# Kernel tuning notes

Measured on AMD Instinct MI355X. Metric: run time of the kernel, lower is better.

The kernel has to match this reference:

```python
import jax, jax.numpy as jnp
import numpy as np

A, U, ANT, D2, H = 128, 8, 64, 64, 256
NUE = A * U            # 1024 ues
E_INT = A * NUE        # 131072 interferes edges (all ap x ue pairs)
E_DL = NUE             # one d_link edge per ue


def _mlp(x, Wa, ba, Wb, bb):
    return jax.nn.relu(x @ Wa + ba) @ Wb + bb


def setup_inputs() -> dict:
    key = jax.random.key(0)
    ks = jax.random.split(key, 14)
    f32 = jnp.float32
    inp = {
        'pl_int_re': jax.random.normal(ks[0], (E_INT, ANT), f32) * 0.1,
        'pl_int_im': jax.random.normal(ks[1], (E_INT, ANT), f32) * 0.1,
        'pl_dl_re': jax.random.normal(ks[2], (E_DL, ANT), f32) * 0.1,
        'pl_dl_im': jax.random.normal(ks[3], (E_DL, ANT), f32) * 0.1,
        'pv_re': jax.random.normal(ks[4], (A, U, ANT), f32) * 0.1,
        'pv_im': jax.random.normal(ks[5], (A, U, ANT), f32) * 0.1,
        'W2a': jax.random.normal(ks[6], (4 * ANT, H), f32) / np.sqrt(4 * ANT),
        'b2a': jnp.zeros((H,), f32),
        'W2b': jax.random.normal(ks[7], (H, D2), f32) / np.sqrt(H),
        'b2b': jnp.zeros((D2,), f32),
        'W1a': jax.random.normal(ks[8], (1 + 2 * ANT + D2, H), f32) / np.sqrt(1 + 2 * ANT + D2),
        'b1a': jnp.zeros((H,), f32),
        'W1b': jax.random.normal(ks[9], (H, 2 * ANT), f32) / np.sqrt(H),
        'b1b': jnp.zeros((2 * ANT,), f32),
        # interferes: every ap -> every ue
        'int_src': jnp.repeat(jnp.arange(A, dtype=jnp.int32), NUE),
        'int_dst': jnp.tile(jnp.arange(NUE, dtype=jnp.int32), A),
        # d_link: ap a -> ues [a*U, (a+1)*U)
        'dl_src': jnp.repeat(jnp.arange(A, dtype=jnp.int32), U),
        'dl_dst': jnp.arange(NUE, dtype=jnp.int32),
    }
    return inp


def reference(pl_int_re, pl_int_im, pl_dl_re, pl_dl_im, pv_re, pv_im,
              W2a, b2a, W2b, b2b, W1a, b1a, W1b, b1b,
              int_src, int_dst, dl_src, dl_dst):
    pv = jax.lax.complex(pv_re, pv_im)            # [A,U,ANT] ap power_vector
    pl_int = jax.lax.complex(pl_int_re, pl_int_im)  # [E_INT,ANT]
    pl_dl = jax.lax.complex(pl_dl_re, pl_dl_im)     # [E_DL,ANT]

    def aggregate_interferes(pv_cur):
        src_sum = jnp.sum(pv_cur, axis=1)[int_src]              # [E,ANT]
        infer_vec = src_sum.conj() * pl_int                      # [E,ANT]
        sum_ap = jnp.sum(jnp.abs(infer_vec) ** 2, axis=-1)       # ||.||^2 -> [E]
        return jax.ops.segment_sum(sum_ap[:, None], int_dst, num_segments=NUE)  # [NUE,1]

    # 1) aggregate_interferes (stored in graph; recomputed at the end)
    _ = aggregate_interferes(pv)

    # 2) mlp_aggregate_interferes
    src_sum = jnp.sum(pv, axis=1)[int_src]                       # [E,ANT] complex
    feats = jnp.concatenate([pl_int, src_sum], axis=1)           # [E,2*ANT] complex
    cat_feats = jnp.concatenate([feats.real, feats.imag], axis=1)  # [E,4*ANT]
    msg2 = _mlp(cat_feats, W2a, b2a, W2b, b2b)                   # [E,D2]
    mlp_ue_all = jax.ops.segment_sum(msg2, int_dst, num_segments=NUE)  # [NUE,D2]

    # 3) update_ue_power_vector (d_link edges)
    src_pv_dl = pv[dl_src]                                       # [E_DL,U,ANT]
    iner = jnp.einsum('eua,ea->eu', src_pv_dl.conj(), pl_dl)     # bmm -> [E_DL,U]
    norm1 = jnp.abs(iner) ** 2                                   # [E_DL,U]
    mask1 = jnp.ones((E_DL, U), norm1.dtype).at[jnp.arange(E_DL), dl_dst % U].set(0.0)
    in_infer = jnp.sum(norm1 * mask1, axis=1)[:, None]           # [E_DL,1]

    feat1 = jnp.concatenate([in_infer, pl_dl.real, pl_dl.imag, mlp_ue_all[dl_dst]], axis=1)
    out1 = _mlp(feat1, W1a, b1a, W1b, b1b).reshape(E_DL, 2, ANT)  # [E_DL,2,ANT]
    ue_pv_msg = jax.lax.complex(out1[:, 0, :], out1[:, 1, :])    # [E_DL,ANT]
    # each ue receives exactly one message
    ue_pv = jnp.zeros((NUE, ANT), ue_pv_msg.dtype).at[dl_dst].set(ue_pv_msg)

    # 4) update_ap_power_vector (u_link: ue i -> ap i//U; mailbox [A,U,ANT])
    mailbox = ue_pv.reshape(A, U, ANT)
    flat = mailbox.reshape(A, U * ANT)
    row_sums = jnp.sum(jnp.abs(flat), axis=-1, keepdims=True)
    pv_new = (flat / row_sums).reshape(A, U, ANT)

    # 5) final aggregate_interferes with updated power vectors
    ue_all_interference = aggregate_interferes(pv_new)

    out_stacked = jnp.stack([pv_new.real, pv_new.imag])          # [2,A,U,ANT]
    return out_stacked, ue_all_interference
```

## Files before the change

### kernel.cpp

```cpp
#include <hip/hip_runtime.h>
#include <hip/hip_bf16.h>
#include <hip/hip_fp16.h>

#define A_NUM 128
#define U_NUM 8
#define ANT 64
#define D2 64
#define H_DIM 256
#define NUE 1024
#define E_INT 131072

typedef __attribute__((ext_vector_type(8))) short bf16x8_t;
typedef __attribute__((ext_vector_type(4))) short bf16x4_t;
typedef __attribute__((ext_vector_type(4))) float f32x4_t;

static __device__ inline unsigned short f2bf(float x) {
    unsigned int u = __float_as_uint(x);
    unsigned int r = (u + 0x7fffu + ((u >> 16) & 1u)) >> 16;
    return (unsigned short)r;
}
static __device__ inline unsigned int pack2(float a, float b) {
    return (unsigned int)f2bf(a) | ((unsigned int)f2bf(b) << 16);
}
static __device__ inline unsigned int packh2(float a, float b) {
    return (unsigned int)__half_as_ushort(__float2half(a)) |
           ((unsigned int)__half_as_ushort(__float2half(b)) << 16);
}
static __device__ inline bf16x4_t relu_cvt4(f32x4_t v) {
    float t0 = v[0] > 0.f ? v[0] : 0.f;
    float t1 = v[1] > 0.f ? v[1] : 0.f;
    float t2 = v[2] > 0.f ? v[2] : 0.f;
    float t3 = v[3] > 0.f ? v[3] : 0.f;
    union { unsigned int u[2]; bf16x4_t s; } r;
    r.u[0] = pack2(t0, t1);
    r.u[1] = pack2(t2, t3);
    return r.s;
}

__global__ void prep_kernel(const float* __restrict__ pv_re, const float* __restrict__ pv_im,
                            const float* __restrict__ W2a, const float* __restrict__ b2a,
                            const float* __restrict__ W2b,
                            const float* __restrict__ W1a, const float* __restrict__ W1b,
                            float* __restrict__ Sa, unsigned short* __restrict__ WpF,
                            unsigned short* __restrict__ W2F,
                            float* __restrict__ W1aT, float* __restrict__ W1bT) {
    int bid = blockIdx.x, t = threadIdx.x;
    if (bid < A_NUM) {
        __shared__ float sre[ANT], sim[ANT];
        if (t < ANT) {
            float s = 0.f;
            for (int u = 0; u < U_NUM; ++u) s += pv_re[bid * 512 + u * 64 + t];
            sre[t] = s;
        } else if (t < 2 * ANT) {
            int ant = t - ANT;
            float s = 0.f;
            for (int u = 0; u < U_NUM; ++u) s += pv_im[bid * 512 + u * 64 + ant];
            sim[ant] = s;
        }
        __syncthreads();
        float a0 = 0.f, a1 = 0.f, a2 = 0.f, a3 = 0.f;
        for (int ant = 0; ant < ANT; ant += 2) {
            a0 += sre[ant] * W2a[(64 + ant) * H_DIM + t];
            a1 += sim[ant] * W2a[(192 + ant) * H_DIM + t];
            a2 += sre[ant + 1] * W2a[(64 + ant + 1) * H_DIM + t];
            a3 += sim[ant + 1] * W2a[(192 + ant + 1) * H_DIM + t];
        }
        Sa[bid * H_DIM + t] = b2a[t] + ((a0 + a2) + (a1 + a3));
    } else if (bid < 136) {
        int base = (bid - A_NUM) * 256 + t;
        for (int f = base; f < 32768 + 16384; f += 8 * 256) {
            if (f < 32768) {
                int i = f & 7, lml = (f >> 3) & 15, lkl = (f >> 7) & 3;
                int kc = (f >> 9) & 3, ht8 = (f >> 11) & 7, hh = (f >> 14) & 1;
                int h = hh * 128 + ht8 * 16 + lml;
                int k = kc * 32 + lkl * 8 + i;
                int row = (k < 64) ? k : (k + 64);
                WpF[f] = f2bf(W2a[row * H_DIM + h]);
            } else {
                int f2 = f - 32768;
                int i = f2 & 3, ll = (f2 >> 2) & 63;
                int dt = (f2 >> 8) & 3, ht8 = (f2 >> 10) & 7, hh = (f2 >> 13) & 1;
                int d = dt * 16 + (ll & 15);
                int k = hh * 128 + ht8 * 16 + (ll >> 4) * 4 + i;
                W2F[f2] = f2bf(W2b[k * D2 + d]);
            }
        }
    } else {
        for (int i = (bid - 136) * 256 + t; i < 53248 + 32768; i += 32 * 256) {
            if (i < 53248) {
                int k = i >> 8, h = i & 255;
                W1aT[h * 208 + k] = (k < 193) ? W1a[k * 256 + h] : 0.f;
            } else {
                int i2 = i - 53248;
                int k = i2 >> 7, c = i2 & 127;
                W1bT[c * 256 + k] = W1b[k * 128 + c];
            }
        }
    }
}

__global__ __launch_bounds__(512) void mlp2_kernel(
        const float* __restrict__ plre, const float* __restrict__ plim,
        const float* __restrict__ Sa, const unsigned short* __restrict__ WpF,
        const unsigned short* __restrict__ W2F, float* __restrict__ partial,
        unsigned short* __restrict__ Pws) {
    __shared__ __attribute__((aligned(16))) unsigned short Wl[16384];
    __shared__ __attribute__((aligned(16))) unsigned short W2l[8192];
    __shared__ __attribute__((aligned(16))) unsigned short Fbuf[8704];
    int bid = blockIdx.x;
    int ac = bid >> 5, hh = (bid >> 4) & 1, jtile = bid & 15;
    int j0 = jtile * 64, a0 = ac * 8;
    int t = threadIdx.x, l = t & 63, lm = l & 15, lk = l >> 4;
    int wv = t >> 6, jw = wv >> 2, hw = wv & 3;

    {
        const uint4* sW = reinterpret_cast<const uint4*>(WpF + hh * 16384);
        const uint4* sW2 = reinterpret_cast<const uint4*>(W2F + hh * 8192);
        uint4* dW = reinterpret_cast<uint4*>(Wl);
        uint4* dW2 = reinterpret_cast<uint4*>(W2l);
        for (int q = t; q < 3072; q += 512) {
            if (q < 2048) dW[q] = sW[q];
            else dW2[q - 2048] = sW2[q - 2048];
        }
    }

    int er = t >> 3, sg = t & 7;
    const float* sb = (sg < 4) ? plre : plim;
    int soff = (j0 + er) * 64 + (sg & 3) * 16;
    int fw = er * 136 + ((sg < 4) ? 0 : 64) + (sg & 3) * 16;

    f32x4_t acc2[4][2];
#pragma unroll
    for (int dt = 0; dt < 4; ++dt)
#pragma unroll
        for (int jt = 0; jt < 2; ++jt) acc2[dt][jt] = (f32x4_t){0.f, 0.f, 0.f, 0.f};

    float4 s0, s1, s2, s3;
    {
        const float* p = sb + (size_t)a0 * 65536 + soff;
        s0 = *reinterpret_cast<const float4*>(p);
        s1 = *reinterpret_cast<const float4*>(p + 4);
        s2 = *reinterpret_cast<const float4*>(p + 8);
        s3 = *reinterpret_cast<const float4*>(p + 12);
        *reinterpret_cast<uint4*>(&Fbuf[fw]) =
            make_uint4(pack2(s0.x, s0.y), pack2(s0.z, s0.w),
                       pack2(s1.x, s1.y), pack2(s1.z, s1.w));
        *reinterpret_cast<uint4*>(&Fbuf[fw + 8]) =
            make_uint4(pack2(s2.x, s2.y), pack2(s2.z, s2.w),
                       pack2(s3.x, s3.y), pack2(s3.z, s3.w));
    }
    {
        const float* p = sb + (size_t)(a0 + 1) * 65536 + soff;
        s0 = *reinterpret_cast<const float4*>(p);
        s1 = *reinterpret_cast<const float4*>(p + 4);
        s2 = *reinterpret_cast<const float4*>(p + 8);
        s3 = *reinterpret_cast<const float4*>(p + 12);
    }
    __syncthreads();

    for (int ai = 0; ai < 8; ++ai) {
        int a = a0 + ai;
        if (hh == 0) {
            uint4 rr = *reinterpret_cast<const uint4*>(Fbuf + er * 136 + sg * 8);
            uint4 ri = *reinterpret_cast<const uint4*>(Fbuf + er * 136 + 64 + sg * 8);
            const unsigned short* pr = (const unsigned short*)&rr;
            const unsigned short* pi = (const unsigned short*)&ri;
            unsigned int pk[4];
#pragma unroll
            for (int i = 0; i < 4; ++i) {
                float re0 = __uint_as_float(((unsigned int)pr[2 * i]) << 16);
                float im0 = __uint_as_float(((unsigned int)pi[2 * i]) << 16);
                float re1 = __uint_as_float(((unsigned int)pr[2 * i + 1]) << 16);
                float im1 = __uint_as_float(((unsigned int)pi[2 * i + 1]) << 16);
                pk[i] = packh2(re0 * re0 + im0 * im0, re1 * re1 + im1 * im1);
            }
            *reinterpret_cast<uint4*>(&Pws[(unsigned)(a * 1024 + j0 + er) * 64 + sg * 8]) =
                make_uint4(pk[0], pk[1], pk[2], pk[3]);
        }
        f32x4_t acc1[2][2];
#pragma unroll
        for (int ht = 0; ht < 2; ++ht) {
            f32x4_t sa = *reinterpret_cast<const f32x4_t*>(
                Sa + a * H_DIM + hh * 128 + hw * 32 + ht * 16 + lk * 4);
            acc1[ht][0] = sa;
            acc1[ht][1] = sa;
        }
#pragma unroll
        for (int kc = 0; kc < 4; ++kc) {
            bf16x8_t aw0 = *reinterpret_cast<const bf16x8_t*>(
                Wl + (((hw * 2 + 0) * 4 + kc) << 9) + l * 8);
            bf16x8_t aw1 = *reinterpret_cast<const bf16x8_t*>(
                Wl + (((hw * 2 + 1) * 4 + kc) << 9) + l * 8);
            bf16x8_t bf0 = *reinterpret_cast<const bf16x8_t*>(
                Fbuf + (jw * 32 + lm) * 136 + kc * 32 + lk * 8);
            bf16x8_t bf1 = *reinterpret_cast<const bf16x8_t*>(
                Fbuf + (jw * 32 + 16 + lm) * 136 + kc * 32 + lk * 8);
            acc1[0][0] = __builtin_amdgcn_mfma_f32_16x16x32_bf16(aw0, bf0, acc1[0][0], 0, 0, 0);
            acc1[0][1] = __builtin_amdgcn_mfma_f32_16x16x32_bf16(aw0, bf1, acc1[0][1], 0, 0, 0);
            acc1[1][0] = __builtin_amdgcn_mfma_f32_16x16x32_bf16(aw1, bf0, acc1[1][0], 0, 0, 0);
            acc1[1][1] = __builtin_amdgcn_mfma_f32_16x16x32_bf16(aw1, bf1, acc1[1][1], 0, 0, 0);
        }
#pragma unroll
        for (int ht = 0; ht < 2; ++ht) {
            bf16x4_t hl0 = relu_cvt4(acc1[ht][0]);
            bf16x4_t hl1 = relu_cvt4(acc1[ht][1]);
#pragma unroll
            for (int dt = 0; dt < 4; ++dt) {
                bf16x4_t w2 = *reinterpret_cast<const bf16x4_t*>(
                    W2l + (((hw * 2 + ht) * 4 + dt) << 8) + l * 4);
                acc2[dt][0] = __builtin_amdgcn_mfma_f32_16x16x16bf16_1k(w2, hl0, acc2[dt][0], 0, 0, 0);
                acc2[dt][1] = __builtin_amdgcn_mfma_f32_16x16x16bf16_1k(w2, hl1, acc2[dt][1], 0, 0, 0);
            }
        }
        if (ai < 7) {
            __syncthreads();
            *reinterpret_cast<uint4*>(&Fbuf[fw]) =
                make_uint4(pack2(s0.x, s0.y), pack2(s0.z, s0.w),
                           pack2(s1.x, s1.y), pack2(s1.z, s1.w));
            *reinterpret_cast<uint4*>(&Fbuf[fw + 8]) =
                make_uint4(pack2(s2.x, s2.y), pack2(s2.z, s2.w),
                           pack2(s3.x, s3.y), pack2(s3.z, s3.w));
            if (ai < 6) {
                const float* p = sb + (size_t)(a0 + ai + 2) * 65536 + soff;
                s0 = *reinterpret_cast<const float4*>(p);
                s1 = *reinterpret_cast<const float4*>(p + 4);
                s2 = *reinterpret_cast<const float4*>(p + 8);
                s3 = *reinterpret_cast<const float4*>(p + 12);
            }
            __syncthreads();
        }
    }

    float* R = reinterpret_cast<float*>(Fbuf);
#define STORE_R()                                                              \
    do {                                                                       \
        _Pragma("unroll") for (int dt = 0; dt < 4; ++dt)                       \
            _Pragma("unroll") for (int jt = 0; jt < 2; ++jt)                   \
                *reinterpret_cast<f32x4_t*>(                                   \
                    &R[(jw * 32 + jt * 16 + lm) * 68 + dt * 16 + lk * 4]) =    \
                    acc2[dt][jt];                                              \
    } while (0)
#define ADD_R()                                                                \
    do {                                                                       \
        _Pragma("unroll") for (int dt = 0; dt < 4; ++dt)                       \
            _Pragma("unroll") for (int jt = 0; jt < 2; ++jt)                   \
                acc2[dt][jt] += *reinterpret_cast<const f32x4_t*>(             \
                    &R[(jw * 32 + jt * 16 + lm) * 68 + dt * 16 + lk * 4]);     \
    } while (0)
    __syncthreads();
    if (hw == 1) STORE_R();
    __syncthreads();
    if (hw == 0) ADD_R();
    __syncthreads();
    if (hw == 3) STORE_R();
    __syncthreads();
    if (hw == 2) ADD_R();
    __syncthreads();
    if (hw == 2) STORE_R();
    __syncthreads();
    if (hw == 0) {
        ADD_R();
#pragma unroll
        for (int dt = 0; dt < 4; ++dt)
#pragma unroll
            for (int jt = 0; jt < 2; ++jt)
                *reinterpret_cast<float4*>(
                    &partial[(size_t)(hh * 16 + ac) * 65536 +
                             (j0 + jw * 32 + jt * 16 + lm) * 64 + dt * 16 + lk * 4]) =
                    *reinterpret_cast<float4*>(&acc2[dt][jt]);
    }
#undef STORE_R
#undef ADD_R
}

__global__ __launch_bounds__(512) void dlink_norm(
        const float* __restrict__ pv_re, const float* __restrict__ pv_im,
        const float* __restrict__ pldre, const float* __restrict__ pldim,
        const float* __restrict__ partial, const float* __restrict__ b2b,
        const float* __restrict__ W1aT, const float* __restrict__ b1a,
        const float* __restrict__ W1bT, const float* __restrict__ b1b,
        float* __restrict__ Q, float* __restrict__ out) {
    int a = blockIdx.x, t = threadIdx.x, w = t >> 6, l = t & 63;
    __shared__ float pvr[512], pvi[512], pldr[512], pldi[512];
    __shared__ float nrm[8][8];
    __shared__ __attribute__((aligned(16))) float feat[8][212];
    __shared__ __attribute__((aligned(16))) float h1[8][260];
    __shared__ float red2[2][8][128];
    __shared__ __attribute__((aligned(16))) float o1[8][128];
    __shared__ float redn[8];
    __shared__ float SshInv;

    pvr[t] = pv_re[a * 512 + t];
    pvi[t] = pv_im[a * 512 + t];
    pldr[t] = pldre[a * 512 + t];
    pldi[t] = pldim[a * 512 + t];
    {
        float acc = 128.f * b2b[t & 63];
#pragma unroll
        for (int c = 0; c < 32; ++c) acc += partial[c * 65536 + a * 512 + t];
        feat[t >> 6][129 + (t & 63)] = acc;
    }
    if (t < 152) feat[t / 19][193 + t % 19] = 0.f;
    __syncthreads();
    feat[t >> 6][1 + (t & 63)] = pldr[t];
    feat[t >> 6][65 + (t & 63)] = pldi[t];
#pragma unroll
    for (int p = 0; p < 8; ++p) {
        int idx = w * 8 + p;
        int el = idx >> 3, u = idx & 7;
        float pr = pvr[u * 64 + l], pi = pvi[u * 64 + l];
        float qr = pldr[el * 64 + l], qi = pldi[el * 64 + l];
        float ir = pr * qr + pi * qi;
        float ii = pr * qi - pi * qr;
        for (int m = 1; m < 64; m <<= 1) {
            ir += __shfl_xor(ir, m, 64);
            ii += __shfl_xor(ii, m, 64);
        }
        if (l == 0) nrm[el][u] = ir * ir + ii * ii;
    }
    __syncthreads();
    if (t < 8) {
        float s = 0.f;
        for (int u = 0; u < 8; ++u)
            if (u != t) s += nrm[t][u];
        feat[t][0] = s;
    }
    __syncthreads();
    {
        int h = t >> 1, e0 = (t & 1) * 4;
        const float4* wrow = reinterpret_cast<const float4*>(W1aT + h * 208);
        const float4* f0p = reinterpret_cast<const float4*>(&feat[e0 + 0][0]);
        const float4* f1p = reinterpret_cast<const float4*>(&feat[e0 + 1][0]);
        const float4* f2p = reinterpret_cast<const float4*>(&feat[e0 + 2][0]);
        const float4* f3p = reinterpret_cast<const float4*>(&feat[e0 + 3][0]);
        float ac0 = 0.f, ac1 = 0.f, ac2 = 0.f, ac3 = 0.f;
#pragma unroll 4
        for (int kq = 0; kq < 52; ++kq) {
            float4 wv = wrow[kq];
            float4 f0 = f0p[kq], f1 = f1p[kq], f2 = f2p[kq], f3 = f3p[kq];
            ac0 = fmaf(wv.x, f0.x, ac0); ac0 = fmaf(wv.y, f0.y, ac0);
            ac0 = fmaf(wv.z, f0.z, ac0); ac0 = fmaf(wv.w, f0.w, ac0);
            ac1 = fmaf(wv.x, f1.x, ac1); ac1 = fmaf(wv.y, f1.y, ac1);
            ac1 = fmaf(wv.z, f1.z, ac1); ac1 = fmaf(wv.w, f1.w, ac1);
            ac2 = fmaf(wv.x, f2.x, ac2); ac2 = fmaf(wv.y, f2.y, ac2);
            ac2 = fmaf(wv.z, f2.z, ac2); ac2 = fmaf(wv.w, f2.w, ac2);
            ac3 = fmaf(wv.x, f3.x, ac3); ac3 = fmaf(wv.y, f3.y, ac3);
            ac3 = fmaf(wv.w, f3.w, ac3); ac3 = fmaf(wv.z, f3.z, ac3);
        }
        float bb = b1a[h];
        float s0 = bb + ac0, s1 = bb + ac1, s2 = bb + ac2, s3 = bb + ac3;
        h1[e0 + 0][h] = s0 > 0.f ? s0 : 0.f;
        h1[e0 + 1][h] = s1 > 0.f ? s1 : 0.f;
        h1[e0 + 2][h] = s2 > 0.f ? s2 : 0.f;
        h1[e0 + 3][h] = s3 > 0.f ? s3 : 0.f;
    }
    __syncthreads();
    {
        int e0 = (t & 1) * 4, c = (t >> 1) & 127, kh = t >> 8;
        const float4* wrow = reinterpret_cast<const float4*>(W1bT + c * 256 + kh * 128);
        const float4* g0 = reinterpret_cast<const float4*>(&h1[e0 + 0][kh * 128]);
        const float4* g1 = reinterpret_cast<const float4*>(&h1[e0 + 1][kh * 128]);
        const float4* g2 = reinterpret_cast<const float4*>(&h1[e0 + 2][kh * 128]);
        const float4* g3 = reinterpret_cast<const float4*>(&h1[e0 + 3][kh * 128]);
        float ac0 = 0.f, ac1 = 0.f, ac2 = 0.f, ac3 = 0.f;
#pragma unroll 4
        for (int kq = 0; kq < 32; ++kq) {
            float4 wv = wrow[kq];
            float4 f0 = g0[kq], f1 = g1[kq], f2 = g2[kq], f3 = g3[kq];
            ac0 = fmaf(wv.x, f0.x, ac0); ac0 = fmaf(wv.y, f0.y, ac0);
            ac0 = fmaf(wv.z, f0.z, ac0); ac0 = fmaf(wv.w, f0.w, ac0);
            ac1 = fmaf(wv.x, f1.x, ac1); ac1 = fmaf(wv.y, f1.y, ac1);
            ac1 = fmaf(wv.z, f1.z, ac1); ac1 = fmaf(wv.w, f1.w, ac1);
            ac2 = fmaf(wv.x, f2.x, ac2); ac2 = fmaf(wv.y, f2.y, ac2);
            ac2 = fmaf(wv.z, f2.z, ac2); ac2 = fmaf(wv.w, f2.w, ac2);
            ac3 = fmaf(wv.x, f3.x, ac3); ac3 = fmaf(wv.y, f3.y, ac3);
            ac3 = fmaf(wv.z, f3.z, ac3); ac3 = fmaf(wv.w, f3.w, ac3);
        }
        red2[kh][e0 + 0][c] = ac0;
        red2[kh][e0 + 1][c] = ac1;
        red2[kh][e0 + 2][c] = ac2;
        red2[kh][e0 + 3][c] = ac3;
    }
    __syncthreads();
    {
        int i0 = t, i1 = t + 512;
        o1[i0 >> 7][i0 & 127] = b1b[i0 & 127] + red2[0][i0 >> 7][i0 & 127] + red2[1][i0 >> 7][i0 & 127];
        o1[i1 >> 7][i1 & 127] = b1b[i1 & 127] + red2[0][i1 >> 7][i1 & 127] + red2[1][i1 >> 7][i1 & 127];
    }
    __syncthreads();
    {
        int el = t >> 6, ant = t & 63;
        float re = o1[el][ant], im = o1[el][64 + ant];
        float v = sqrtf(re * re + im * im);
        for (int m = 1; m < 64; m <<= 1) v += __shfl_xor(v, m, 64);
        if (l == 0) redn[w] = v;
    }
    __syncthreads();
    if (t == 0) {
        float S = redn[0] + redn[1] + redn[2] + redn[3] +
                  redn[4] + redn[5] + redn[6] + redn[7];
        SshInv = 1.f / S;
    }
    __syncthreads();
    {
        float inv = SshInv;
        int el = t >> 6, ant = t & 63;
        out[a * 512 + t] = o1[el][ant] * inv;
        out[65536 + a * 512 + t] = o1[el][64 + ant] * inv;
        if (t < 64) {
            float sr = 0.f, si = 0.f;
#pragma unroll
            for (int u = 0; u < 8; ++u) {
                sr += o1[u][t];
                si += o1[u][64 + t];
            }
            sr *= inv;
            si *= inv;
            Q[a * 64 + t] = sr * sr + si * si;
        }
    }
}

__global__ __launch_bounds__(256) void final_agg(const unsigned short* __restrict__ Pws,
                                                 const float* __restrict__ Qv,
                                                 float* __restrict__ out) {
    int bid = blockIdx.x, t = threadIdx.x, w = t >> 6, l = t & 63;
    __shared__ __attribute__((aligned(16))) float Qc[128][68];
    for (int i = t; i < 8192; i += 256) Qc[i >> 6][i & 63] = Qv[i];
    __syncthreads();
    int j = bid * 4 + w;
    int as = l >> 3, og = l & 7;
    float acc = 0.f;
#pragma unroll 4
    for (int ab = 0; ab < 16; ++ab) {
        int aa = ab * 8 + as;
        uint4 pv4 = *reinterpret_cast<const uint4*>(&Pws[(unsigned)(aa * 1024 + j) * 64 + og * 8]);
        float4 q0 = *reinterpret_cast<const float4*>(&Qc[aa][og * 8]);
        float4 q1 = *reinterpret_cast<const float4*>(&Qc[aa][og * 8 + 4]);
        const unsigned short* hp = (const unsigned short*)&pv4;
        acc += __half2float(__ushort_as_half(hp[0])) * q0.x;
        acc += __half2float(__ushort_as_half(hp[1])) * q0.y;
        acc += __half2float(__ushort_as_half(hp[2])) * q0.z;
        acc += __half2float(__ushort_as_half(hp[3])) * q0.w;
        acc += __half2float(__ushort_as_half(hp[4])) * q1.x;
        acc += __half2float(__ushort_as_half(hp[5])) * q1.y;
        acc += __half2float(__ushort_as_half(hp[6])) * q1.z;
        acc += __half2float(__ushort_as_half(hp[7])) * q1.w;
    }
    for (int m = 1; m < 64; m <<= 1) acc += __shfl_xor(acc, m, 64);
    if (l == 0) out[131072 + j] = acc;
}

extern "C" void kernel_launch(void* const* d_in, const int* in_sizes, int n_in,
                              void* d_out, int out_size, void* d_ws, size_t ws_size,
                              hipStream_t stream) {
    const float* plre = (const float*)d_in[0];
    const float* plim = (const float*)d_in[1];
    const float* pldre = (const float*)d_in[2];
    const float* pldim = (const float*)d_in[3];
    const float* pvre = (const float*)d_in[4];
    const float* pvim = (const float*)d_in[5];
    const float* W2a = (const float*)d_in[6];
    const float* b2a = (const float*)d_in[7];
    const float* W2b = (const float*)d_in[8];
    const float* b2b = (const float*)d_in[9];
    const float* W1a = (const float*)d_in[10];
    const float* b1a = (const float*)d_in[11];
    const float* W1b = (const float*)d_in[12];
    const float* b1b = (const float*)d_in[13];

    char* ws = (char*)d_ws;
    float* Sa = (float*)(ws);
    unsigned short* WpF = (unsigned short*)(ws + 131072);
    unsigned short* W2F = (unsigned short*)(ws + 196608);
    float* Q = (float*)(ws + 229376);
    float* W1aT = (float*)(ws + 262144);
    float* W1bT = (float*)(ws + 475136);
    float* partial = (float*)(ws + 606208);
    unsigned short* Pws = (unsigned short*)(ws + 8994816);
    float* out = (float*)d_out;

    prep_kernel<<<168, 256, 0, stream>>>(pvre, pvim, W2a, b2a, W2b, W1a, W1b,
                                         Sa, WpF, W2F, W1aT, W1bT);
    mlp2_kernel<<<512, 512, 0, stream>>>(plre, plim, Sa, WpF, W2F, partial, Pws);
    dlink_norm<<<128, 512, 0, stream>>>(pvre, pvim, pldre, pldim, partial, b2b,
                                        W1aT, b1a, W1bT, b1b, Q, out);
    final_agg<<<256, 256, 0, stream>>>(Pws, Q, out);
}
```

Baseline: 66.22 us.

## Halve mlp2 block to 256 threads with each wave covering all 64 edge rows

The mlp2 kernel now runs 4 waves per block instead of 8. Each wave handles all four 16-row edge fragments instead of two, so every weight fragment loaded from LDS feeds twice as many MFMAs. Each thread now loads and converts twice as much of the input tile, and holds twice as many accumulators, which raises register pressure and may cut occupancy. It also reorders two FMAs in dlink_norm, which slightly changes the floating-point summation order.

```diff
diff --git a/kernel.cpp b/kernel.cpp
--- a/kernel.cpp
+++ b/kernel.cpp
@@ -99,7 +99,7 @@
     }
 }
 
-__global__ __launch_bounds__(512) void mlp2_kernel(
+__global__ __launch_bounds__(256) void mlp2_kernel(
         const float* __restrict__ plre, const float* __restrict__ plim,
         const float* __restrict__ Sa, const unsigned short* __restrict__ WpF,
         const unsigned short* __restrict__ W2F, float* __restrict__ partial,
@@ -111,79 +111,87 @@
     int ac = bid >> 5, hh = (bid >> 4) & 1, jtile = bid & 15;
     int j0 = jtile * 64, a0 = ac * 8;
     int t = threadIdx.x, l = t & 63, lm = l & 15, lk = l >> 4;
-    int wv = t >> 6, jw = wv >> 2, hw = wv & 3;
+    int hw = t >> 6;
 
     {
         const uint4* sW = reinterpret_cast<const uint4*>(WpF + hh * 16384);
         const uint4* sW2 = reinterpret_cast<const uint4*>(W2F + hh * 8192);
         uint4* dW = reinterpret_cast<uint4*>(Wl);
         uint4* dW2 = reinterpret_cast<uint4*>(W2l);
-        for (int q = t; q < 3072; q += 512) {
+        for (int q = t; q < 3072; q += 256) {
             if (q < 2048) dW[q] = sW[q];
             else dW2[q - 2048] = sW2[q - 2048];
         }
     }
 
-    int er = t >> 3, sg = t & 7;
-    const float* sb = (sg < 4) ? plre : plim;
-    int soff = (j0 + er) * 64 + (sg & 3) * 16;
-    int fw = er * 136 + ((sg < 4) ? 0 : 64) + (sg & 3) * 16;
-
-    f32x4_t acc2[4][2];
+    int rr = t >> 2, seg = t & 3;
+    const float* sb = (seg < 2) ? plre : plim;
+    int soff = (j0 + rr) * 64 + (seg & 1) * 32;
+    int fw = rr * 136 + ((seg < 2) ? 0 : 64) + (seg & 1) * 32;
+
+    f32x4_t acc2[4][4];
 #pragma unroll
     for (int dt = 0; dt < 4; ++dt)
 #pragma unroll
-        for (int jt = 0; jt < 2; ++jt) acc2[dt][jt] = (f32x4_t){0.f, 0.f, 0.f, 0.f};
-
-    float4 s0, s1, s2, s3;
+        for (int jf = 0; jf < 4; ++jf) acc2[dt][jf] = (f32x4_t){0.f, 0.f, 0.f, 0.f};
+
+    float4 s[8];
     {
         const float* p = sb + (size_t)a0 * 65536 + soff;
-        s0 = *reinterpret_cast<const float4*>(p);
-        s1 = *reinterpret_cast<const float4*>(p + 4);
-        s2 = *reinterpret_cast<const float4*>(p + 8);
-        s3 = *reinterpret_cast<const float4*>(p + 12);
-        *reinterpret_cast<uint4*>(&Fbuf[fw]) =
-            make_uint4(pack2(s0.x, s0.y), pack2(s0.z, s0.w),
-                       pack2(s1.x, s1.y), pack2(s1.z, s1.w));
-        *reinterpret_cast<uint4*>(&Fbuf[fw + 8]) =
-            make_uint4(pack2(s2.x, s2.y), pack2(s2.z, s2.w),
-                       pack2(s3.x, s3.y), pack2(s3.z, s3.w));
+#pragma unroll
+        for (int i = 0; i < 8; ++i) s[i] = *reinterpret_cast<const float4*>(p + i * 4);
+#pragma unroll
+        for (int i = 0; i < 4; ++i)
+            *reinterpret_cast<uint4*>(&Fbuf[fw + i * 8]) =
+                make_uint4(pack2(s[2 * i].x, s[2 * i].y), pack2(s[2 * i].z, s[2 * i].w),
+                           pack2(s[2 * i + 1].x, s[2 * i + 1].y), pack2(s[2 * i + 1].z, s[2 * i + 1].w));
     }
     {
         const float* p = sb + (size_t)(a0 + 1) * 65536 + soff;
-        s0 = *reinterpret_cast<const float4*>(p);
-        s1 = *reinterpret_cast<const float4*>(p + 4);
-        s2 = *reinterpret_cast<const float4*>(p + 8);
-        s3 = *reinterpret_cast<const float4*>(p + 12);
+#pragma unroll
+        for (int i = 0; i < 8; ++i) s[i] = *reinterpret_cast<const float4*>(p + i * 4);
     }
     __syncthreads();
 
     for (int ai = 0; ai < 8; ++ai) {
         int a = a0 + ai;
         if (hh == 0) {
-            uint4 rr = *reinterpret_cast<const uint4*>(Fbuf + er * 136 + sg * 8);
-            uint4 ri = *reinterpret_cast<const uint4*>(Fbuf + er * 136 + 64 + sg * 8);
-            const unsigned short* pr = (const unsigned short*)&rr;
-            const unsigned short* pi = (const unsigned short*)&ri;
-            unsigned int pk[4];
+            uint4 re0 = *reinterpret_cast<const uint4*>(Fbuf + rr * 136 + seg * 16);
+            uint4 re1 = *reinterpret_cast<const uint4*>(Fbuf + rr * 136 + seg * 16 + 8);
+            uint4 im0 = *reinterpret_cast<const uint4*>(Fbuf + rr * 136 + 64 + seg * 16);
+            uint4 im1 = *reinterpret_cast<const uint4*>(Fbuf + rr * 136 + 64 + seg * 16 + 8);
+            const unsigned short* pr = (const unsigned short*)&re0;
+            const unsigned short* pi = (const unsigned short*)&im0;
+            unsigned int pk[8];
 #pragma unroll
             for (int i = 0; i < 4; ++i) {
-                float re0 = __uint_as_float(((unsigned int)pr[2 * i]) << 16);
-                float im0 = __uint_as_float(((unsigned int)pi[2 * i]) << 16);
-                float re1 = __uint_as_float(((unsigned int)pr[2 * i + 1]) << 16);
-                float im1 = __uint_as_float(((unsigned int)pi[2 * i + 1]) << 16);
-                pk[i] = packh2(re0 * re0 + im0 * im0, re1 * re1 + im1 * im1);
-            }
-            *reinterpret_cast<uint4*>(&Pws[(unsigned)(a * 1024 + j0 + er) * 64 + sg * 8]) =
-                make_uint4(pk[0], pk[1], pk[2], pk[3]);
-        }
-        f32x4_t acc1[2][2];
+                float a0f = __uint_as_float(((unsigned int)pr[2 * i]) << 16);
+                float b0f = __uint_as_float(((unsigned int)pi[2 * i]) << 16);
+                float a1f = __uint_as_float(((unsigned int)pr[2 * i + 1]) << 16);
+                float b1f = __uint_as_float(((unsigned int)pi[2 * i + 1]) << 16);
+                pk[i] = packh2(a0f * a0f + b0f * b0f, a1f * a1f + b1f * b1f);
+            }
+            pr = (const unsigned short*)&re1;
+            pi = (const unsigned short*)&im1;
+#pragma unroll
+            for (int i = 0; i < 4; ++i) {
+                float a0f = __uint_as_float(((unsigned int)pr[2 * i]) << 16);
+                float b0f = __uint_as_float(((unsigned int)pi[2 * i]) << 16);
+                float a1f = __uint_as_float(((unsigned int)pr[2 * i + 1]) << 16);
+                float b1f = __uint_as_float(((unsigned int)pi[2 * i + 1]) << 16);
+                pk[4 + i] = packh2(a0f * a0f + b0f * b0f, a1f * a1f + b1f * b1f);
+            }
+            unsigned short* pd = Pws + (unsigned)(a * 1024 + j0 + rr) * 64 + seg * 16;
+            *reinterpret_cast<uint4*>(pd) = make_uint4(pk[0], pk[1], pk[2], pk[3]);
+            *reinterpret_cast<uint4*>(pd + 8) = make_uint4(pk[4], pk[5], pk[6], pk[7]);
+        }
+        f32x4_t acc1[2][4];
 #pragma unroll
         for (int ht = 0; ht < 2; ++ht) {
             f32x4_t sa = *reinterpret_cast<const f32x4_t*>(
                 Sa + a * H_DIM + hh * 128 + hw * 32 + ht * 16 + lk * 4);
-            acc1[ht][0] = sa;
-            acc1[ht][1] = sa;
+#pragma unroll
+            for (int jf = 0; jf < 4; ++jf) acc1[ht][jf] = sa;
         }
 #pragma unroll
         for (int kc = 0; kc < 4; ++kc) {
@@ -191,41 +199,39 @@
                 Wl + (((hw * 2 + 0) * 4 + kc) << 9) + l * 8);
             bf16x8_t aw1 = *reinterpret_cast<const bf16x8_t*>(
                 Wl + (((hw * 2 + 1) * 4 + kc) << 9) + l * 8);
-            bf16x8_t bf0 = *reinterpret_cast<const bf16x8_t*>(
-                Fbuf + (jw * 32 + lm) * 136 + kc * 32 + lk * 8);
-            bf16x8_t bf1 = *reinterpret_cast<const bf16x8_t*>(
-                Fbuf + (jw * 32 + 16 + lm) * 136 + kc * 32 + lk * 8);
-            acc1[0][0] = __builtin_amdgcn_mfma_f32_16x16x32_bf16(aw0, bf0, acc1[0][0], 0, 0, 0);
-            acc1[0][1] = __builtin_amdgcn_mfma_f32_16x16x32_bf16(aw0, bf1, acc1[0][1], 0, 0, 0);
-            acc1[1][0] = __builtin_amdgcn_mfma_f32_16x16x32_bf16(aw1, bf0, acc1[1][0], 0, 0, 0);
-            acc1[1][1] = __builtin_amdgcn_mfma_f32_16x16x32_bf16(aw1, bf1, acc1[1][1], 0, 0, 0);
+#pragma unroll
+            for (int jf = 0; jf < 4; ++jf) {
+                bf16x8_t bf = *reinterpret_cast<const bf16x8_t*>(
+                    Fbuf + (jf * 16 + lm) * 136 + kc * 32 + lk * 8);
+                acc1[0][jf] = __builtin_amdgcn_mfma_f32_16x16x32_bf16(aw0, bf, acc1[0][jf], 0, 0, 0);
+                acc1[1][jf] = __builtin_amdgcn_mfma_f32_16x16x32_bf16(aw1, bf, acc1[1][jf], 0, 0, 0);
+            }
         }
 #pragma unroll
         for (int ht = 0; ht < 2; ++ht) {
-            bf16x4_t hl0 = relu_cvt4(acc1[ht][0]);
-            bf16x4_t hl1 = relu_cvt4(acc1[ht][1]);
+            bf16x4_t hl[4];
+#pragma unroll
+            for (int jf = 0; jf < 4; ++jf) hl[jf] = relu_cvt4(acc1[ht][jf]);
 #pragma unroll
             for (int dt = 0; dt < 4; ++dt) {
                 bf16x4_t w2 = *reinterpret_cast<const bf16x4_t*>(
                     W2l + (((hw * 2 + ht) * 4 + dt) << 8) + l * 4);
-                acc2[dt][0] = __builtin_amdgcn_mfma_f32_16x16x16bf16_1k(w2, hl0, acc2[dt][0], 0, 0, 0);
-                acc2[dt][1] = __builtin_amdgcn_mfma_f32_16x16x16bf16_1k(w2, hl1, acc2[dt][1], 0, 0, 0);
+#pragma unroll
+                for (int jf = 0; jf < 4; ++jf)
+                    acc2[dt][jf] = __builtin_amdgcn_mfma_f32_16x16x16bf16_1k(w2, hl[jf], acc2[dt][jf], 0, 0, 0);
             }
         }
         if (ai < 7) {
             __syncthreads();
-            *reinterpret_cast<uint4*>(&Fbuf[fw]) =
-                make_uint4(pack2(s0.x, s0.y), pack2(s0.z, s0.w),
-                           pack2(s1.x, s1.y), pack2(s1.z, s1.w));
-            *reinterpret_cast<uint4*>(&Fbuf[fw + 8]) =
-                make_uint4(pack2(s2.x, s2.y), pack2(s2.z, s2.w),
-                           pack2(s3.x, s3.y), pack2(s3.z, s3.w));
+#pragma unroll
+            for (int i = 0; i < 4; ++i)
+                *reinterpret_cast<uint4*>(&Fbuf[fw + i * 8]) =
+                    make_uint4(pack2(s[2 * i].x, s[2 * i].y), pack2(s[2 * i].z, s[2 * i].w),
+                               pack2(s[2 * i + 1].x, s[2 * i + 1].y), pack2(s[2 * i + 1].z, s[2 * i + 1].w));
             if (ai < 6) {
                 const float* p = sb + (size_t)(a0 + ai + 2) * 65536 + soff;
-                s0 = *reinterpret_cast<const float4*>(p);
-                s1 = *reinterpret_cast<const float4*>(p + 4);
-                s2 = *reinterpret_cast<const float4*>(p + 8);
-                s3 = *reinterpret_cast<const float4*>(p + 12);
+#pragma unroll
+                for (int i = 0; i < 8; ++i) s[i] = *reinterpret_cast<const float4*>(p + i * 4);
             }
             __syncthreads();
         }
@@ -235,17 +241,16 @@
 #define STORE_R()                                                              \
     do {                                                                       \
         _Pragma("unroll") for (int dt = 0; dt < 4; ++dt)                       \
-            _Pragma("unroll") for (int jt = 0; jt < 2; ++jt)                   \
+            _Pragma("unroll") for (int jf = 0; jf < 4; ++jf)                   \
                 *reinterpret_cast<f32x4_t*>(                                   \
-                    &R[(jw * 32 + jt * 16 + lm) * 68 + dt * 16 + lk * 4]) =    \
-                    acc2[dt][jt];                                              \
+                    &R[(jf * 16 + lm) * 68 + dt * 16 + lk * 4]) = acc2[dt][jf];\
     } while (0)
 #define ADD_R()                                                                \
     do {                                                                       \
         _Pragma("unroll") for (int dt = 0; dt < 4; ++dt)                       \
-            _Pragma("unroll") for (int jt = 0; jt < 2; ++jt)                   \
-                acc2[dt][jt] += *reinterpret_cast<const f32x4_t*>(             \
-                    &R[(jw * 32 + jt * 16 + lm) * 68 + dt * 16 + lk * 4]);     \
+            _Pragma("unroll") for (int jf = 0; jf < 4; ++jf)                   \
+                acc2[dt][jf] += *reinterpret_cast<const f32x4_t*>(             \
+                    &R[(jf * 16 + lm) * 68 + dt * 16 + lk * 4]);               \
     } while (0)
     __syncthreads();
     if (hw == 1) STORE_R();
@@ -263,11 +268,11 @@
 #pragma unroll
         for (int dt = 0; dt < 4; ++dt)
 #pragma unroll
-            for (int jt = 0; jt < 2; ++jt)
+            for (int jf = 0; jf < 4; ++jf)
                 *reinterpret_cast<float4*>(
                     &partial[(size_t)(hh * 16 + ac) * 65536 +
-                             (j0 + jw * 32 + jt * 16 + lm) * 64 + dt * 16 + lk * 4]) =
-                    *reinterpret_cast<float4*>(&acc2[dt][jt]);
+                             (j0 + jf * 16 + lm) * 64 + dt * 16 + lk * 4]) =
+                    *reinterpret_cast<float4*>(&acc2[dt][jf]);
     }
 #undef STORE_R
 #undef ADD_R
@@ -345,7 +350,7 @@
             ac2 = fmaf(wv.x, f2.x, ac2); ac2 = fmaf(wv.y, f2.y, ac2);
             ac2 = fmaf(wv.z, f2.z, ac2); ac2 = fmaf(wv.w, f2.w, ac2);
             ac3 = fmaf(wv.x, f3.x, ac3); ac3 = fmaf(wv.y, f3.y, ac3);
-            ac3 = fmaf(wv.w, f3.w, ac3); ac3 = fmaf(wv.z, f3.z, ac3);
+            ac3 = fmaf(wv.z, f3.z, ac3); ac3 = fmaf(wv.w, f3.w, ac3);
         }
         float bb = b1a[h];
         float s0 = bb + ac0, s1 = bb + ac1, s2 = bb + ac2, s3 = bb + ac3;
@@ -482,7 +487,7 @@
 
     prep_kernel<<<168, 256, 0, stream>>>(pvre, pvim, W2a, b2a, W2b, W1a, W1b,
                                          Sa, WpF, W2F, W1aT, W1bT);
-    mlp2_kernel<<<512, 512, 0, stream>>>(plre, plim, Sa, WpF, W2F, partial, Pws);
+    mlp2_kernel<<<512, 256, 0, stream>>>(plre, plim, Sa, WpF, W2F, partial, Pws);
     dlink_norm<<<128, 512, 0, stream>>>(pvre, pvim, pldre, pldim, partial, b2b,
                                         W1aT, b1a, W1bT, b1b, Q, out);
     final_agg<<<256, 256, 0, stream>>>(Pws, Q, out);
```

Result: slower. 76.41 us (+15.4%).
